# Kernel optimization log

Hardware: AMD Instinct MI355X
Metric: run time of the kernel (lower is better)

The kernel has to match this reference:

```python
import jax, jax.numpy as jnp
import numpy as np

HEADS = 4
HEAD_SIZE = 100
SCALE = 1.0 / (100.0 ** 0.5)  # original divides by 100**0.5


def setup_inputs() -> dict:
    key = jax.random.key(0)
    ks = jax.random.split(key, 8)
    B, L, D = 16, 2048, 400
    u0, u1 = 512, 256
    return {
        "x": jax.random.normal(ks[0], (B, L, D), dtype=jnp.float32),
        "kernel": jax.random.normal(ks[1], (3, D, HEAD_SIZE), dtype=jnp.float32) * 0.05,
        "dense": jax.random.normal(ks[2], (D, 400), dtype=jnp.float32) * 0.05,
        "w2": jax.random.normal(ks[3], (400, 400), dtype=jnp.float32) * 0.05,
        "b2": jnp.zeros((400,), dtype=jnp.float32),
        "w3": jax.random.normal(ks[4], (800, u0), dtype=jnp.float32) * 0.05,
        "b3": jnp.zeros((u0,), dtype=jnp.float32),
        "w4": jax.random.normal(ks[5], (u0, u1), dtype=jnp.float32) * 0.05,
        "b4": jnp.zeros((u1,), dtype=jnp.float32),
    }


def reference(x, kernel, dense, w2, b2, w3, b3, w4, b4):
    # --- MultiHeadAttention(4, 100): all heads share the same kernel, so
    # compute one head and tile (identical math to the per-head Python loop).
    q = jnp.einsum("bld,dh->blh", x, kernel[0])  # [B,L,100]
    k = jnp.einsum("bld,dh->blh", x, kernel[1])
    v = jnp.einsum("bld,dh->blh", x, kernel[2])
    scores = jnp.einsum("bqh,bkh->bqk", q, k) * SCALE  # [B,L,L]
    attn = jax.nn.softmax(scores, axis=-1)
    head = jnp.einsum("bqk,bkh->bqh", attn, v)  # [B,L,100]
    out = jnp.concatenate([head] * HEADS, axis=-1)  # [B,L,400]
    out = jnp.einsum("blh,ho->blo", out, dense)  # [B,L,400]
    # Dropout(0.1): identity at inference.
    h = jax.nn.relu(jnp.einsum("blo,ou->blu", out, w2) + b2)  # [B,L,400]
    h_max = jnp.max(h, axis=1)   # GlobalMaxPooling1D -> [B,400]
    h_avg = jnp.mean(h, axis=1)  # GlobalAveragePooling1D -> [B,400]
    z = jnp.concatenate([h_max, h_avg], axis=-1)  # [B,800]
    z = jax.nn.relu(z @ w3 + b3)
    z = jax.nn.relu(z @ w4 + b4)
    return z
```

## Files before the change

kernel.cpp:

```cpp
#include <hip/hip_runtime.h>


#define L_SEQ 2048
#define HS    100
#define ATT_SCALE 0.1f

typedef __attribute__((ext_vector_type(8))) short bf16x8;
typedef __attribute__((ext_vector_type(4))) float f32x4;
#define MFMA16 __builtin_amdgcn_mfma_f32_16x16x32_bf16

__device__ __forceinline__ ushort f2bf(float f) {
    unsigned u = __float_as_uint(f);
    u += 0x7fffu + ((u >> 16) & 1u);
    return (ushort)(u >> 16);
}
__device__ __forceinline__ float bfval(ushort u) {
    return __uint_as_float((unsigned)u << 16);
}

__global__ __launch_bounds__(256)
void k_w(const float* __restrict__ dense, const float* __restrict__ w2,
         ushort* __restrict__ WT_hi, ushort* __restrict__ WT_lo) {
    __shared__ float rows[4 * 400];
    __shared__ float red[4][4][64];
    const int cb = blockIdx.x;
    const int r0 = blockIdx.y * 4;
    const int tid = threadIdx.x;
    const int c = tid & 63, kk = tid >> 6;
    const int col = cb * 64 + c;
    for (int i = tid; i < 1600; i += 256) {
        int rr = r0 + i / 400, cc = i - (i / 400) * 400;
        rows[i] = (rr < 100)
            ? dense[rr * 400 + cc] + dense[(rr + 100) * 400 + cc]
              + dense[(rr + 200) * 400 + cc] + dense[(rr + 300) * 400 + cc]
            : 0.f;
    }
    __syncthreads();
    float a0 = 0.f, a1 = 0.f, a2 = 0.f, a3 = 0.f;
    if (col < 400) {
        const int kbase = kk * 100;
#pragma unroll 4
        for (int k = 0; k < 100; ++k) {
            float wv = w2[(kbase + k) * 400 + col];
            a0 += rows[kbase + k] * wv;
            a1 += rows[400 + kbase + k] * wv;
            a2 += rows[800 + kbase + k] * wv;
            a3 += rows[1200 + kbase + k] * wv;
        }
    }
    red[kk][0][c] = a0; red[kk][1][c] = a1; red[kk][2][c] = a2; red[kk][3][c] = a3;
    __syncthreads();
    {
        const int r = kk;
        float s = red[0][r][c] + red[1][r][c] + red[2][r][c] + red[3][r][c];
        ushort hi = f2bf(s);
        WT_hi[col * 128 + r0 + r] = hi;
        WT_lo[col * 128 + r0 + r] = f2bf(s - bfval(hi));
    }
}

__global__ __launch_bounds__(448)
void k_wprep(const float* __restrict__ kw,
             ushort* __restrict__ wT_hi, ushort* __restrict__ wT_lo) {
    const int j = blockIdx.x;
    const int c = j >> 7, h = j & 127;
    const int k = threadIdx.x;
    float v = 0.f;
    if (h < 100 && k < 400) v = kw[c * 40000 + k * 100 + h];
    if (c == 0) v *= ATT_SCALE;
    ushort hi = f2bf(v);
    wT_hi[(size_t)j * 448 + k] = hi;
    wT_lo[(size_t)j * 448 + k] = f2bf(v - bfval(hi));
}

__global__ __launch_bounds__(512, 2)
void k_qkv(const float* __restrict__ x,
           const ushort* __restrict__ wT_hi, const ushort* __restrict__ wT_lo,
           ushort* __restrict__ q_hi, ushort* __restrict__ q_lo,
           ushort* __restrict__ k_hi, ushort* __restrict__ vT)
{
    __shared__ __align__(16) ushort xh_s[2][128 * 64];
    __shared__ __align__(16) ushort xl_s[2][128 * 64];
    const int row0 = blockIdx.x << 7;
    const int bb = row0 >> 11;
    const int tid = threadIdx.x;
    const int lane = tid & 63, wv = tid >> 6;
    const int q15 = lane & 15, g0 = lane >> 4;
    const int cW = (wv & 3) * 96, rW = (wv >> 2) * 64;

    f32x4 acc[6][4];
#pragma unroll
    for (int mf = 0; mf < 6; ++mf)
#pragma unroll
        for (int nf = 0; nf < 4; ++nf) acc[mf][nf] = (f32x4){0.f, 0.f, 0.f, 0.f};

    float4 st[4];
#define QKV_STAGE_LOAD(KC)                                                     \
    _Pragma("unroll") for (int i = 0; i < 4; ++i) {                            \
        int idx = tid + i * 512; int r = idx >> 4, c4 = idx & 15;              \
        int g = (KC) * 64 + c4 * 4;                                            \
        st[i] = (g <= 396) ? *reinterpret_cast<const float4*>(                 \
                                 &x[(size_t)(row0 + r) * 400 + g])             \
                           : make_float4(0.f, 0.f, 0.f, 0.f);                  \
    }
#define QKV_STAGE_WRITE(BUF)                                                   \
    _Pragma("unroll") for (int i = 0; i < 4; ++i) {                            \
        int idx = tid + i * 512; int r = idx >> 4, c4 = idx & 15;              \
        ushort4 hi4, lo4;                                                      \
        hi4.x = f2bf(st[i].x); lo4.x = f2bf(st[i].x - bfval(hi4.x));           \
        hi4.y = f2bf(st[i].y); lo4.y = f2bf(st[i].y - bfval(hi4.y));           \
        hi4.z = f2bf(st[i].z); lo4.z = f2bf(st[i].z - bfval(hi4.z));           \
        hi4.w = f2bf(st[i].w); lo4.w = f2bf(st[i].w - bfval(hi4.w));           \
        int off = r * 128 + ((c4 * 8) ^ ((r & 7) << 4));                       \
        *reinterpret_cast<ushort4*>((char*)xh_s[BUF] + off) = hi4;             \
        *reinterpret_cast<ushort4*>((char*)xl_s[BUF] + off) = lo4;             \
    }

    QKV_STAGE_LOAD(0)

    for (int kc = 0; kc < 7; ++kc) {
        const int cur = kc & 1;
        QKV_STAGE_WRITE(cur)
        if (kc < 6) { QKV_STAGE_LOAD(kc + 1) }
        __syncthreads();
#pragma unroll
        for (int k2 = 0; k2 < 2; ++k2) {
            const int k0 = kc * 64 + k2 * 32;
            bf16x8 bh[4], bl[4];
#pragma unroll
            for (int nf = 0; nf < 4; ++nf) {
                int row = rW + nf * 16 + q15;
                int boff = row * 128 + ((k2 * 64 + g0 * 16) ^ ((row & 7) << 4));
                bh[nf] = *reinterpret_cast<const bf16x8*>((char*)xh_s[cur] + boff);
                bl[nf] = *reinterpret_cast<const bf16x8*>((char*)xl_s[cur] + boff);
            }
#pragma unroll
            for (int mf = 0; mf < 6; ++mf) {
                int col = cW + mf * 16 + q15;
                bf16x8 ah = *reinterpret_cast<const bf16x8*>(
                    wT_hi + (size_t)col * 448 + k0 + g0 * 8);
                bf16x8 al = *reinterpret_cast<const bf16x8*>(
                    wT_lo + (size_t)col * 448 + k0 + g0 * 8);
#pragma unroll
                for (int nf = 0; nf < 4; ++nf) {
                    acc[mf][nf] = MFMA16(ah, bh[nf], acc[mf][nf], 0, 0, 0);
                    acc[mf][nf] = MFMA16(ah, bl[nf], acc[mf][nf], 0, 0, 0);
                    acc[mf][nf] = MFMA16(al, bh[nf], acc[mf][nf], 0, 0, 0);
                }
            }
        }
    }

#pragma unroll
    for (int mf = 0; mf < 6; ++mf) {
        const int col0 = cW + mf * 16 + 4 * g0;
        const int c = col0 >> 7, h0 = col0 & 127;
#pragma unroll
        for (int nf = 0; nf < 4; ++nf) {
            const size_t row = (size_t)(row0 + rW + nf * 16 + q15);
            if (c == 0) {
                ushort4 hi4, lo4;
#pragma unroll
                for (int r = 0; r < 4; ++r) {
                    float vf = acc[mf][nf][r];
                    ushort h = f2bf(vf);
                    ((ushort*)&hi4)[r] = h;
                    ((ushort*)&lo4)[r] = f2bf(vf - bfval(h));
                }
                *reinterpret_cast<ushort4*>(&q_hi[row * 128 + h0]) = hi4;
                *reinterpret_cast<ushort4*>(&q_lo[row * 128 + h0]) = lo4;
            } else if (c == 1) {
                ushort4 hi4;
#pragma unroll
                for (int r = 0; r < 4; ++r) ((ushort*)&hi4)[r] = f2bf(acc[mf][nf][r]);
                *reinterpret_cast<ushort4*>(&k_hi[row * 128 + h0]) = hi4;
            } else {
                const int keyl = (int)row & 2047;
#pragma unroll
                for (int jj = 0; jj < 4; ++jj) {
                    int h = h0 + jj;
                    if (h < 100)
                        vT[((size_t)bb * 112 + h) * 2048 + keyl] = f2bf(acc[mf][nf][jj]);
                }
            }
        }
    }
#undef QKV_STAGE_LOAD
#undef QKV_STAGE_WRITE
}

template<bool PART>
__global__ __launch_bounds__(256, 4)
void k_flashT(const ushort* __restrict__ q_hi, const ushort* __restrict__ q_lo,
              const ushort* __restrict__ k_hi, const ushort* __restrict__ vT,
              float* __restrict__ outp, float2* __restrict__ mlP)
{
    __shared__ __align__(16) ushort k_s[64 * 128];
    __shared__ __align__(16) ushort vT_s[112 * 64];
    __shared__ __align__(16) ushort p_s[4][16 * 64];

    const int id = blockIdx.x;
    int b, qt, part;
    if (PART) {
        const int Lg = (id & 7) * 128 + (id >> 3);
        b = Lg >> 6; const int rem = Lg & 63; qt = rem >> 1; part = rem & 1;
    } else {
        const int Lg = (id & 7) * 64 + (id >> 3);
        b = Lg >> 5; qt = Lg & 31; part = 0;
    }
    const int q0 = qt * 64;
    const size_t bL = (size_t)b * L_SEQ;
    const int ktBeg = part * 16, ktEnd = PART ? ktBeg + 16 : 32;

    const int tid = threadIdx.x;
    const int lane = tid & 63, wv = tid >> 6;
    const int q15 = lane & 15, g0 = lane >> 4;

    bf16x8 qhf[4], qlf[4];
    {
        const ushort* qr = q_hi + (bL + q0 + 16 * wv + q15) * 128 + 8 * g0;
        const ushort* qs = q_lo + (bL + q0 + 16 * wv + q15) * 128 + 8 * g0;
#pragma unroll
        for (int kh = 0; kh < 4; ++kh) {
            qhf[kh] = *reinterpret_cast<const bf16x8*>(qr + 32 * kh);
            qlf[kh] = *reinterpret_cast<const bf16x8*>(qs + 32 * kh);
        }
    }

    float m_run = -1e30f, l_run = 0.f;
    f32x4 acc[7];
#pragma unroll
    for (int ht = 0; ht < 7; ++ht) acc[ht] = (f32x4){0.f, 0.f, 0.f, 0.f};

    for (int kt = ktBeg; kt < ktEnd; ++kt) {
        const int kb = kt * 64;
        __syncthreads();
        {
            const char* khg = (const char*)(k_hi + (bL + kb) * 128);
            for (int n = tid; n < 1024; n += 256) {
                int key = n >> 4, gg = n & 15;
                uint4 d = *reinterpret_cast<const uint4*>(khg + n * 16);
                *reinterpret_cast<uint4*>((char*)k_s + key * 256 + (((gg ^ (key & 15))) << 4)) = d;
            }
            const char* vtg = (const char*)(vT + (size_t)b * 112 * 2048) + kb * 2;
            for (int n = tid; n < 896; n += 256) {
                int h = n >> 3, gg = n & 7;
                uint4 d = *reinterpret_cast<const uint4*>(vtg + h * 4096 + gg * 16);
                *reinterpret_cast<uint4*>((char*)vT_s + h * 128 + (((gg ^ (h & 7))) << 4)) = d;
            }
        }
        __syncthreads();

        f32x4 sacc[4];
        const int kx = q15 << 4;
#pragma unroll
        for (int t = 0; t < 4; ++t) {
            sacc[t] = (f32x4){0.f, 0.f, 0.f, 0.f};
            const char* kr = (const char*)k_s + (t * 16 + q15) * 256;
#pragma unroll
            for (int kh = 0; kh < 4; ++kh) {
                bf16x8 kf = *reinterpret_cast<const bf16x8*>(kr + ((((kh << 2) + g0) << 4) ^ kx));
                sacc[t] = MFMA16(kf, qhf[kh], sacc[t], 0, 0, 0);
                sacc[t] = MFMA16(kf, qlf[kh], sacc[t], 0, 0, 0);
            }
        }

        float mxl = -1e30f;
#pragma unroll
        for (int t = 0; t < 4; ++t)
#pragma unroll
            for (int r = 0; r < 4; ++r) mxl = fmaxf(mxl, sacc[t][r]);
        mxl = fmaxf(mxl, __shfl_xor(mxl, 16));
        mxl = fmaxf(mxl, __shfl_xor(mxl, 32));
        if (!__all(mxl - m_run <= 8.f)) {
            float mn = fmaxf(m_run, mxl);
            float alpha = __expf(m_run - mn);
            l_run *= alpha;
            m_run = mn;
            float alv[4];
#pragma unroll
            for (int r = 0; r < 4; ++r) alv[r] = __shfl(alpha, (g0 << 2) | r);
#pragma unroll
            for (int ht = 0; ht < 7; ++ht)
#pragma unroll
                for (int r = 0; r < 4; ++r) acc[ht][r] *= alv[r];
        }
        float lsum = 0.f;
        float p[4][4];
#pragma unroll
        for (int t = 0; t < 4; ++t)
#pragma unroll
            for (int r = 0; r < 4; ++r) {
                p[t][r] = __expf(sacc[t][r] - m_run);
                lsum += p[t][r];
            }
        lsum += __shfl_xor(lsum, 16);
        lsum += __shfl_xor(lsum, 32);
        l_run += lsum;

        ushort* pw = p_s[wv];
        const int qb = q15 * 128;
#pragma unroll
        for (int t = 0; t < 4; ++t) {
            ushort4 pv4;
            pv4.x = f2bf(p[t][0]); pv4.y = f2bf(p[t][1]);
            pv4.z = f2bf(p[t][2]); pv4.w = f2bf(p[t][3]);
            int gw = (t << 1) + (g0 >> 1);
            *reinterpret_cast<ushort4*>((char*)pw + qb + (((gw ^ (q15 & 7))) << 4)
                                        + ((g0 & 1) << 3)) = pv4;
        }

        bf16x8 pa0 = *reinterpret_cast<const bf16x8*>((char*)pw + qb + (((g0 ^ (q15 & 7))) << 4));
        bf16x8 pa1 = *reinterpret_cast<const bf16x8*>((char*)pw + qb + ((((4 + g0) ^ (q15 & 7))) << 4));
#pragma unroll
        for (int ht = 0; ht < 7; ++ht) {
            const char* vr = (const char*)vT_s + (ht * 16 + q15) * 128;
            const int hx = ((ht * 16 + q15) & 7) << 4;
            bf16x8 vb0 = *reinterpret_cast<const bf16x8*>(vr + ((g0 << 4) ^ hx));
            bf16x8 vb1 = *reinterpret_cast<const bf16x8*>(vr + (((4 + g0) << 4) ^ hx));
            acc[ht] = MFMA16(pa0, vb0, acc[ht], 0, 0, 0);
            acc[ht] = MFMA16(pa1, vb1, acc[ht], 0, 0, 0);
        }
    }

    if (PART) {
        float* ap = outp + (size_t)part * 3276800
                    + (bL + q0 + 16 * wv + (g0 << 2)) * 100;
#pragma unroll
        for (int ht = 0; ht < 7; ++ht) {
            int col = ht * 16 + q15;
            if (col < 100) {
#pragma unroll
                for (int r = 0; r < 4; ++r) ap[r * 100 + col] = acc[ht][r];
            }
        }
        if (g0 == 0) {
            float2 ml; ml.x = m_run; ml.y = l_run;
            mlP[(size_t)part * 32768 + bL + q0 + 16 * wv + q15] = ml;
        }
    } else {
        float linv[4];
#pragma unroll
        for (int r = 0; r < 4; ++r) linv[r] = 1.0f / __shfl(l_run, (g0 << 2) | r);
#pragma unroll
        for (int ht = 0; ht < 7; ++ht) {
            int col = ht * 16 + q15;
            if (col < 100) {
                float* hp = outp + (bL + q0 + 16 * wv + (g0 << 2)) * 100 + col;
#pragma unroll
                for (int r = 0; r < 4; ++r) hp[r * 100] = acc[ht][r] * linv[r];
            }
        }
    }
}

__global__ __launch_bounds__(256)
void k_combine(float* __restrict__ accP, const float2* __restrict__ mlP)
{
    int g = blockIdx.x * 256 + threadIdx.x;
    if (g < 32768 * 25) {
        int row = g / 25, c4 = g - row * 25;
        float2 ml1 = mlP[row], ml2 = mlP[32768 + row];
        float M = fmaxf(ml1.x, ml2.x);
        float w1 = __expf(ml1.x - M), w2 = __expf(ml2.x - M);
        float inv = 1.0f / (w1 * ml1.y + w2 * ml2.y);
        float4 a1 = *reinterpret_cast<const float4*>(&accP[(size_t)row * 100 + c4 * 4]);
        float4 a2 = *reinterpret_cast<const float4*>(&accP[3276800 + (size_t)row * 100 + c4 * 4]);
        float4 o;
        o.x = (w1 * a1.x + w2 * a2.x) * inv;
        o.y = (w1 * a1.y + w2 * a2.y) * inv;
        o.z = (w1 * a1.z + w2 * a2.z) * inv;
        o.w = (w1 * a1.w + w2 * a2.w) * inv;
        *reinterpret_cast<float4*>(&accP[(size_t)row * 100 + c4 * 4]) = o;
    }
}

__global__ __launch_bounds__(512, 2)
void k_hpool(const float* __restrict__ head,
             const ushort* __restrict__ WT_hi, const ushort* __restrict__ WT_lo,
             const float* __restrict__ b2,
             float* __restrict__ pmax, float* __restrict__ psum)
{
    __shared__ __align__(16) ushort hh_s[128 * 128];
    __shared__ __align__(16) ushort hl_s[128 * 128];
    __shared__ float pm_s[8][112], ps_s[8][112];
    const int blk = blockIdx.x;
    const int row0 = blk << 7;
    const int tid = threadIdx.x;
    const int lane = tid & 63, wv = tid >> 6;
    const int q15 = lane & 15, g0 = lane >> 4;
    const int wvM = wv >> 2, wvN = wv & 3;

    for (int i = 0; i < 7; ++i) {
        int idx = tid + i * 512;
        if (idx < 3200) {
            int r = idx / 25, cc = idx - r * 25;
            float4 t = *reinterpret_cast<const float4*>(
                &head[(size_t)(row0 + r) * 100 + cc * 4]);
            ushort4 hi4, lo4;
            hi4.x = f2bf(t.x); lo4.x = f2bf(t.x - bfval(hi4.x));
            hi4.y = f2bf(t.y); lo4.y = f2bf(t.y - bfval(hi4.y));
            hi4.z = f2bf(t.z); lo4.z = f2bf(t.z - bfval(hi4.z));
            hi4.w = f2bf(t.w); lo4.w = f2bf(t.w - bfval(hi4.w));
            int off = r * 256 + ((cc * 8) ^ ((r & 7) << 4));
            *reinterpret_cast<ushort4*>((char*)hh_s + off) = hi4;
            *reinterpret_cast<ushort4*>((char*)hl_s + off) = lo4;
        }
    }
    for (int idx = tid; idx < 896; idx += 512) {
        int r = idx / 7, c7 = idx - (idx / 7) * 7;
        int off = r * 256 + (((200 + c7 * 8)) ^ ((r & 7) << 4));
        ushort4 z = {0, 0, 0, 0};
        *reinterpret_cast<ushort4*>((char*)hh_s + off) = z;
        *reinterpret_cast<ushort4*>((char*)hl_s + off) = z;
    }
    __syncthreads();

    f32x4 acc[4][7];
#pragma unroll
    for (int mf = 0; mf < 4; ++mf)
#pragma unroll
        for (int nf = 0; nf < 7; ++nf) acc[mf][nf] = (f32x4){0.f, 0.f, 0.f, 0.f};

#pragma unroll
    for (int ks = 0; ks < 4; ++ks) {
        const int k0 = ks * 32;
        bf16x8 ah[4], al[4];
#pragma unroll
        for (int mf = 0; mf < 4; ++mf) {
            int rowL = wvM * 64 + mf * 16 + q15;
            int aoff = rowL * 256 + ((k0 * 2 + g0 * 16) ^ ((rowL & 7) << 4));
            ah[mf] = *reinterpret_cast<const bf16x8*>((char*)hh_s + aoff);
            al[mf] = *reinterpret_cast<const bf16x8*>((char*)hl_s + aoff);
        }
#pragma unroll
        for (int nf = 0; nf < 7; ++nf) {
            int col = wvN * 112 + nf * 16 + q15;
            bf16x8 bh = *reinterpret_cast<const bf16x8*>(WT_hi + col * 128 + k0 + g0 * 8);
            bf16x8 bl = *reinterpret_cast<const bf16x8*>(WT_lo + col * 128 + k0 + g0 * 8);
#pragma unroll
            for (int mf = 0; mf < 4; ++mf) {
                acc[mf][nf] = MFMA16(ah[mf], bh, acc[mf][nf], 0, 0, 0);
                acc[mf][nf] = MFMA16(ah[mf], bl, acc[mf][nf], 0, 0, 0);
                acc[mf][nf] = MFMA16(al[mf], bh, acc[mf][nf], 0, 0, 0);
            }
        }
    }

#pragma unroll
    for (int nf = 0; nf < 7; ++nf) {
        int col = wvN * 112 + nf * 16 + q15;
        float bv = (col < 400) ? b2[col] : 0.f;
        float mx = 0.f, sm = 0.f;
#pragma unroll
        for (int mf = 0; mf < 4; ++mf)
#pragma unroll
            for (int r = 0; r < 4; ++r) {
                float hv = fmaxf(acc[mf][nf][r] + bv, 0.f);
                mx = fmaxf(mx, hv); sm += hv;
            }
        mx = fmaxf(mx, __shfl_xor(mx, 16));
        mx = fmaxf(mx, __shfl_xor(mx, 32));
        sm += __shfl_xor(sm, 16);
        sm += __shfl_xor(sm, 32);
        if (g0 == 0) {
            pm_s[wv][nf * 16 + q15] = mx;
            ps_s[wv][nf * 16 + q15] = sm;
        }
    }
    __syncthreads();
    if (tid < 448) {
        int wn = tid / 112, cc = tid - wn * 112;
        float mx = fmaxf(pm_s[wn][cc], pm_s[4 + wn][cc]);
        float sm = ps_s[wn][cc] + ps_s[4 + wn][cc];
        if (tid < 400) {
            pmax[blk * 400 + tid] = mx;
            psum[blk * 400 + tid] = sm;
        }
    }
}

__global__ __launch_bounds__(512)
void k_reduce(const float* __restrict__ pmax, const float* __restrict__ psum,
              float* __restrict__ zin)
{
    const int b = blockIdx.x, c = threadIdx.x;
    if (c < 400) {
        float m = 0.f, s = 0.f;
#pragma unroll
        for (int tt = 0; tt < 16; ++tt) {
            m = fmaxf(m, pmax[(b * 16 + tt) * 400 + c]);
            s += psum[(b * 16 + tt) * 400 + c];
        }
        zin[b * 800 + c] = m;
        zin[b * 800 + 400 + c] = s * (1.0f / 2048.0f);
    }
}

__global__ __launch_bounds__(512)
void k_mlp1(const float* __restrict__ zin, const float* __restrict__ w3,
            const float* __restrict__ b3, float* __restrict__ z1)
{
    __shared__ float zs[800];
    __shared__ float red[8][64];
    const int cb = blockIdx.x, b = blockIdx.y;
    const int tid = threadIdx.x;
    const int c = tid & 63, kk = tid >> 6;
    const int col = cb * 64 + c;
    for (int i = tid; i < 800; i += 512) zs[i] = zin[b * 800 + i];
    __syncthreads();
    float acc = 0.f;
    const int k0 = kk * 100;
#pragma unroll 4
    for (int k = 0; k < 100; ++k)
        acc += zs[k0 + k] * w3[(k0 + k) * 512 + col];
    red[kk][c] = acc;
    __syncthreads();
    if (kk == 0) {
        float a = b3[col];
#pragma unroll
        for (int g = 0; g < 8; ++g) a += red[g][c];
        z1[b * 512 + col] = fmaxf(a, 0.f);
    }
}

__global__ __launch_bounds__(512)
void k_mlp2(const float* __restrict__ z1, const float* __restrict__ w4,
            const float* __restrict__ b4, float* __restrict__ out)
{
    __shared__ float zs[512];
    __shared__ float red[8][64];
    const int cb = blockIdx.x, b = blockIdx.y;
    const int tid = threadIdx.x;
    const int c = tid & 63, kk = tid >> 6;
    const int col = cb * 64 + c;
    if (tid < 512) zs[tid] = z1[b * 512 + tid];
    __syncthreads();
    float acc = 0.f;
    const int k0 = kk * 64;
#pragma unroll 4
    for (int k = 0; k < 64; ++k)
        acc += zs[k0 + k] * w4[(k0 + k) * 256 + col];
    red[kk][c] = acc;
    __syncthreads();
    if (kk == 0) {
        float a = b4[col];
#pragma unroll
        for (int g = 0; g < 8; ++g) a += red[g][c];
        out[b * 256 + col] = fmaxf(a, 0.f);
    }
}

extern "C" void kernel_launch(void* const* d_in, const int* in_sizes, int n_in,
                              void* d_out, int out_size, void* d_ws, size_t ws_size,
                              hipStream_t stream) {
    (void)in_sizes; (void)n_in; (void)out_size;
    const float* x     = (const float*)d_in[0];
    const float* kw    = (const float*)d_in[1];
    const float* dense = (const float*)d_in[2];
    const float* w2    = (const float*)d_in[3];
    const float* b2    = (const float*)d_in[4];
    const float* w3    = (const float*)d_in[5];
    const float* b3    = (const float*)d_in[6];
    const float* w4    = (const float*)d_in[7];
    const float* b4    = (const float*)d_in[8];
    float* ws = (float*)d_ws;
    ushort* q_hi = (ushort*)(ws);
    ushort* q_lo = (ushort*)(ws + 2097152);
    ushort* k_hi = (ushort*)(ws + 4194304);
    ushort* vT   = (ushort*)(ws + 6291456);
    float*  head = ws + 8126464;
    ushort* wT_hi = (ushort*)(ws + 8126464);
    ushort* wT_lo = (ushort*)(ws + 8212480);
    float*  pmax = ws;
    float*  psum = ws + 2097152;
    float*  zin  = ws + 4194304;
    float*  z1   = ws + 4207104;
    float*  outp = (float*)d_out;

    const bool split = ws_size >= (size_t)14999552 * sizeof(float);
    float*  accP  = head;
    float2* mlP   = (float2*)(ws + 14680064);
    ushort* WT_hi = (ushort*)(ws + (split ? 14942208 : 11403264));
    ushort* WT_lo = WT_hi + 57344;

    k_w     <<<dim3(7, 32),    dim3(256), 0, stream>>>(dense, w2, WT_hi, WT_lo);
    k_wprep <<<dim3(384),      dim3(448), 0, stream>>>(kw, wT_hi, wT_lo);
    k_qkv   <<<dim3(256),      dim3(512), 0, stream>>>(x, wT_hi, wT_lo,
                                                       q_hi, q_lo, k_hi, vT);
    if (split) {
        k_flashT<true> <<<dim3(1024), dim3(256), 0, stream>>>(q_hi, q_lo, k_hi, vT,
                                                              accP, mlP);
        k_combine      <<<dim3(3200), dim3(256), 0, stream>>>(accP, mlP);
    } else {
        k_flashT<false><<<dim3(512),  dim3(256), 0, stream>>>(q_hi, q_lo, k_hi, vT,
                                                              head, nullptr);
    }
    k_hpool <<<dim3(256),      dim3(512), 0, stream>>>(head, WT_hi, WT_lo, b2,
                                                       pmax, psum);
    k_reduce<<<dim3(16),       dim3(512), 0, stream>>>(pmax, psum, zin);
    k_mlp1  <<<dim3(8, 16),    dim3(512), 0, stream>>>(zin, w3, b3, z1);
    k_mlp2  <<<dim3(4, 16),    dim3(512), 0, stream>>>(z1, w4, b4, outp);
}
```

Measured before the change: 197.0 us.

## Fuse split-KV combine into pooling kernel and use exp2 softmax with setprio

Folds log2(e) into the Q weight scale so softmax can call the hardware v_exp_f32 (exp2) directly, and raises the deferred-rescale threshold to match the base-2 domain. The bf16 packing of probabilities switches to v_cvt_pk_bf16_f32, and s_setprio is raised around the MFMA blocks. The separate combine kernel is removed and its merge of the two partial attention results is done inside the hpool load stage. This drops one launch and a full read/write pass over the head tensor, at the cost of extra loads in hpool and rounding behaviour that differs slightly from the original.

```diff
diff --git a/kernel.cpp b/kernel.cpp
--- a/kernel.cpp
+++ b/kernel.cpp
@@ -3,7 +3,8 @@
 
 #define L_SEQ 2048
 #define HS    100
-#define ATT_SCALE 0.1f
+#define ATT_SCALE_L2E 0.14426950408889634f
+#define DEFER_THR 11.5416f
 
 typedef __attribute__((ext_vector_type(8))) short bf16x8;
 typedef __attribute__((ext_vector_type(4))) float f32x4;
@@ -16,6 +17,11 @@
 }
 __device__ __forceinline__ float bfval(ushort u) {
     return __uint_as_float((unsigned)u << 16);
+}
+__device__ __forceinline__ float exp2_hw(float x) {
+    float r;
+    asm("v_exp_f32 %0, %1" : "=v"(r) : "v"(x));
+    return r;
 }
 
 __global__ __launch_bounds__(256)
@@ -67,7 +73,7 @@
     const int k = threadIdx.x;
     float v = 0.f;
     if (h < 100 && k < 400) v = kw[c * 40000 + k * 100 + h];
-    if (c == 0) v *= ATT_SCALE;
+    if (c == 0) v *= ATT_SCALE_L2E;
     ushort hi = f2bf(v);
     wT_hi[(size_t)j * 448 + k] = hi;
     wT_lo[(size_t)j * 448 + k] = f2bf(v - bfval(hi));
@@ -253,6 +259,7 @@
 
         f32x4 sacc[4];
         const int kx = q15 << 4;
+        __builtin_amdgcn_s_setprio(1);
 #pragma unroll
         for (int t = 0; t < 4; ++t) {
             sacc[t] = (f32x4){0.f, 0.f, 0.f, 0.f};
@@ -264,6 +271,7 @@
                 sacc[t] = MFMA16(kf, qlf[kh], sacc[t], 0, 0, 0);
             }
         }
+        __builtin_amdgcn_s_setprio(0);
 
         float mxl = -1e30f;
 #pragma unroll
@@ -272,9 +280,9 @@
             for (int r = 0; r < 4; ++r) mxl = fmaxf(mxl, sacc[t][r]);
         mxl = fmaxf(mxl, __shfl_xor(mxl, 16));
         mxl = fmaxf(mxl, __shfl_xor(mxl, 32));
-        if (!__all(mxl - m_run <= 8.f)) {
+        if (!__all(mxl - m_run <= DEFER_THR)) {
             float mn = fmaxf(m_run, mxl);
-            float alpha = __expf(m_run - mn);
+            float alpha = exp2_hw(m_run - mn);
             l_run *= alpha;
             m_run = mn;
             float alv[4];
@@ -291,7 +299,7 @@
         for (int t = 0; t < 4; ++t)
 #pragma unroll
             for (int r = 0; r < 4; ++r) {
-                p[t][r] = __expf(sacc[t][r] - m_run);
+                p[t][r] = exp2_hw(sacc[t][r] - m_run);
                 lsum += p[t][r];
             }
         lsum += __shfl_xor(lsum, 16);
@@ -302,16 +310,17 @@
         const int qb = q15 * 128;
 #pragma unroll
         for (int t = 0; t < 4; ++t) {
-            ushort4 pv4;
-            pv4.x = f2bf(p[t][0]); pv4.y = f2bf(p[t][1]);
-            pv4.z = f2bf(p[t][2]); pv4.w = f2bf(p[t][3]);
+            uint2 pv;
+            asm("v_cvt_pk_bf16_f32 %0, %1, %2" : "=v"(pv.x) : "v"(p[t][0]), "v"(p[t][1]));
+            asm("v_cvt_pk_bf16_f32 %0, %1, %2" : "=v"(pv.y) : "v"(p[t][2]), "v"(p[t][3]));
             int gw = (t << 1) + (g0 >> 1);
-            *reinterpret_cast<ushort4*>((char*)pw + qb + (((gw ^ (q15 & 7))) << 4)
-                                        + ((g0 & 1) << 3)) = pv4;
+            *reinterpret_cast<uint2*>((char*)pw + qb + (((gw ^ (q15 & 7))) << 4)
+                                      + ((g0 & 1) << 3)) = pv;
         }
 
         bf16x8 pa0 = *reinterpret_cast<const bf16x8*>((char*)pw + qb + (((g0 ^ (q15 & 7))) << 4));
         bf16x8 pa1 = *reinterpret_cast<const bf16x8*>((char*)pw + qb + ((((4 + g0) ^ (q15 & 7))) << 4));
+        __builtin_amdgcn_s_setprio(1);
 #pragma unroll
         for (int ht = 0; ht < 7; ++ht) {
             const char* vr = (const char*)vT_s + (ht * 16 + q15) * 128;
@@ -321,6 +330,7 @@
             acc[ht] = MFMA16(pa0, vb0, acc[ht], 0, 0, 0);
             acc[ht] = MFMA16(pa1, vb1, acc[ht], 0, 0, 0);
         }
+        __builtin_amdgcn_s_setprio(0);
     }
 
     if (PART) {
@@ -354,32 +364,12 @@
     }
 }
 
-__global__ __launch_bounds__(256)
-void k_combine(float* __restrict__ accP, const float2* __restrict__ mlP)
-{
-    int g = blockIdx.x * 256 + threadIdx.x;
-    if (g < 32768 * 25) {
-        int row = g / 25, c4 = g - row * 25;
-        float2 ml1 = mlP[row], ml2 = mlP[32768 + row];
-        float M = fmaxf(ml1.x, ml2.x);
-        float w1 = __expf(ml1.x - M), w2 = __expf(ml2.x - M);
-        float inv = 1.0f / (w1 * ml1.y + w2 * ml2.y);
-        float4 a1 = *reinterpret_cast<const float4*>(&accP[(size_t)row * 100 + c4 * 4]);
-        float4 a2 = *reinterpret_cast<const float4*>(&accP[3276800 + (size_t)row * 100 + c4 * 4]);
-        float4 o;
-        o.x = (w1 * a1.x + w2 * a2.x) * inv;
-        o.y = (w1 * a1.y + w2 * a2.y) * inv;
-        o.z = (w1 * a1.z + w2 * a2.z) * inv;
-        o.w = (w1 * a1.w + w2 * a2.w) * inv;
-        *reinterpret_cast<float4*>(&accP[(size_t)row * 100 + c4 * 4]) = o;
-    }
-}
-
+template<bool COMBINE>
 __global__ __launch_bounds__(512, 2)
-void k_hpool(const float* __restrict__ head,
-             const ushort* __restrict__ WT_hi, const ushort* __restrict__ WT_lo,
-             const float* __restrict__ b2,
-             float* __restrict__ pmax, float* __restrict__ psum)
+void k_hpoolT(const float* __restrict__ accP, const float2* __restrict__ mlP,
+              const ushort* __restrict__ WT_hi, const ushort* __restrict__ WT_lo,
+              const float* __restrict__ b2,
+              float* __restrict__ pmax, float* __restrict__ psum)
 {
     __shared__ __align__(16) ushort hh_s[128 * 128];
     __shared__ __align__(16) ushort hl_s[128 * 128];
@@ -395,8 +385,23 @@
         int idx = tid + i * 512;
         if (idx < 3200) {
             int r = idx / 25, cc = idx - r * 25;
-            float4 t = *reinterpret_cast<const float4*>(
-                &head[(size_t)(row0 + r) * 100 + cc * 4]);
+            const size_t row = (size_t)(row0 + r);
+            float4 t;
+            if (COMBINE) {
+                float2 ml1 = mlP[row], ml2 = mlP[32768 + row];
+                float M = fmaxf(ml1.x, ml2.x);
+                float w1 = exp2_hw(ml1.x - M), w2 = exp2_hw(ml2.x - M);
+                float inv = 1.0f / (w1 * ml1.y + w2 * ml2.y);
+                w1 *= inv; w2 *= inv;
+                float4 a1 = *reinterpret_cast<const float4*>(&accP[row * 100 + cc * 4]);
+                float4 a2 = *reinterpret_cast<const float4*>(&accP[3276800 + row * 100 + cc * 4]);
+                t.x = w1 * a1.x + w2 * a2.x;
+                t.y = w1 * a1.y + w2 * a2.y;
+                t.z = w1 * a1.z + w2 * a2.z;
+                t.w = w1 * a1.w + w2 * a2.w;
+            } else {
+                t = *reinterpret_cast<const float4*>(&accP[row * 100 + cc * 4]);
+            }
             ushort4 hi4, lo4;
             hi4.x = f2bf(t.x); lo4.x = f2bf(t.x - bfval(hi4.x));
             hi4.y = f2bf(t.y); lo4.y = f2bf(t.y - bfval(hi4.y));
@@ -589,15 +594,18 @@
     k_qkv   <<<dim3(256),      dim3(512), 0, stream>>>(x, wT_hi, wT_lo,
                                                        q_hi, q_lo, k_hi, vT);
     if (split) {
-        k_flashT<true> <<<dim3(1024), dim3(256), 0, stream>>>(q_hi, q_lo, k_hi, vT,
-                                                              accP, mlP);
-        k_combine      <<<dim3(3200), dim3(256), 0, stream>>>(accP, mlP);
+        k_flashT<true>  <<<dim3(1024), dim3(256), 0, stream>>>(q_hi, q_lo, k_hi, vT,
+                                                               accP, mlP);
+        k_hpoolT<true>  <<<dim3(256),  dim3(512), 0, stream>>>(accP, mlP,
+                                                               WT_hi, WT_lo, b2,
+                                                               pmax, psum);
     } else {
-        k_flashT<false><<<dim3(512),  dim3(256), 0, stream>>>(q_hi, q_lo, k_hi, vT,
-                                                              head, nullptr);
-    }
-    k_hpool <<<dim3(256),      dim3(512), 0, stream>>>(head, WT_hi, WT_lo, b2,
-                                                       pmax, psum);
+        k_flashT<false> <<<dim3(512),  dim3(256), 0, stream>>>(q_hi, q_lo, k_hi, vT,
+                                                               head, nullptr);
+        k_hpoolT<false> <<<dim3(256),  dim3(512), 0, stream>>>(head, nullptr,
+                                                               WT_hi, WT_lo, b2,
+                                                               pmax, psum);
+    }
     k_reduce<<<dim3(16),       dim3(512), 0, stream>>>(pmax, psum, zin);
     k_mlp1  <<<dim3(8, 16),    dim3(512), 0, stream>>>(zin, w3, b3, z1);
     k_mlp2  <<<dim3(4, 16),    dim3(512), 0, stream>>>(z1, w4, b4, outp);
```

New measurement: 189.4 us. 1.04x faster.
